# Kernel tuning notes

Hardware: AMD Instinct MI355X
Metric: run time of the kernel (lower is better)

Reference implementation:

```python
import jax, jax.numpy as jnp
import numpy as np

N_STREAMS = 4
DIM = 256
TMAX = 20
RMS_EPS = 1e-05
SK_EPS = 1e-08


def sinkhorn_knopp(logits):
    # logits: [B, T, n, n]; tmax fixed iterations of row/col normalization
    x = logits.astype(jnp.float32)
    x = x - jnp.max(x, axis=(-2, -1), keepdims=True)
    x = jnp.exp(x)
    for _ in range(TMAX):
        x = x / (jnp.sum(x, axis=-2, keepdims=True) + SK_EPS)
        x = x / (jnp.sum(x, axis=-1, keepdims=True) + SK_EPS)
    return x.astype(logits.dtype)


def setup_inputs() -> dict:
    key = jax.random.key(0)
    ks = jax.random.split(key, 5)
    B, T, n, C = 8, 4096, N_STREAMS, DIM
    nc = n * C
    x_streams = jax.random.normal(ks[0], (B, T, n, C), dtype=jnp.float32)
    scale = jnp.ones((nc,), dtype=jnp.float32)
    lim = 1.0 / np.sqrt(nc)
    w_pre = jax.random.uniform(ks[1], (n, nc), minval=-lim, maxval=lim, dtype=jnp.float32)
    w_post = jax.random.uniform(ks[2], (n, nc), minval=-lim, maxval=lim, dtype=jnp.float32)
    w_res = jax.random.uniform(ks[3], (n * n, nc), minval=-lim, maxval=lim, dtype=jnp.float32)
    return {
        "x_streams": x_streams,
        "scale": scale,
        "w_pre": w_pre,
        "w_post": w_post,
        "w_res": w_res,
        "alpha_pre": jnp.float32(0.01),
        "alpha_post": jnp.float32(0.01),
        "alpha_res": jnp.float32(0.01),
        "b_pre": jnp.zeros((n,), dtype=jnp.float32),
        "b_post": jnp.zeros((n,), dtype=jnp.float32),
        "b_res": jnp.zeros((n * n,), dtype=jnp.float32),
    }


def reference(x_streams, scale, w_pre, w_post, w_res,
              alpha_pre, alpha_post, alpha_res, b_pre, b_post, b_res):
    B, T, n, C = x_streams.shape
    x_flat = x_streams.reshape(B, T, n * C)
    # RMSNorm over flattened stream dim
    rms = jnp.mean(x_flat * x_flat, axis=-1, keepdims=True)
    x_norm = x_flat * jax.lax.rsqrt(rms + RMS_EPS) * scale
    # routing projections (Linear with no bias == x @ W.T)
    h_pre = jax.nn.sigmoid(alpha_pre * (x_norm @ w_pre.T) + b_pre)          # [B,T,n]
    h_post = 2.0 * jax.nn.sigmoid(alpha_post * (x_norm @ w_post.T) + b_post)  # [B,T,n]
    h_res = (alpha_res * (x_norm @ w_res.T) + b_res).reshape(B, T, n, n)
    h_res = sinkhorn_knopp(h_res)
    # mixing
    x_in = jnp.einsum('btn,btnc->btc', h_pre, x_streams)   # pre-mix (residual = Identity)
    y = x_in
    resmix = jnp.einsum('btij,btjc->btic', h_res, x_streams)
    addy = h_post[..., None] * y[..., None, :]
    return resmix + addy
```

## Files before the change

kernel.cpp:

```cpp
#include <hip/hip_runtime.h>
#include <math.h>

#define G 16

__device__ __forceinline__ float sigmoidf_(float s) {
    return 1.0f / (1.0f + __expf(-s));
}

__device__ __forceinline__ float fold_(float X, float Y, int m, int l) {
    const bool hi = (l & m) != 0;
    const float a = hi ? Y : X;
    const float b = hi ? X : Y;
    return a + __shfl_xor(b, m);
}

__global__ __launch_bounds__(256, 2)
void fused_route_mix(const float* __restrict__ x,
                     const float* __restrict__ scale,
                     const float* __restrict__ w_pre,
                     const float* __restrict__ w_post,
                     const float* __restrict__ w_res,
                     const float* __restrict__ ap_p,
                     const float* __restrict__ apo_p,
                     const float* __restrict__ ar_p,
                     const float* __restrict__ b_pre,
                     const float* __restrict__ b_post,
                     const float* __restrict__ b_res,
                     float* __restrict__ out,
                     int rounds)
{
    __shared__ __align__(16) float xs[G * 1024];
    __shared__ float hraw[G * 24];
    __shared__ float sslds[G];
    __shared__ __align__(16) float Mlds[G * 16];

    const int t = threadIdx.x;
    const int w = t >> 6;
    const int l = t & 63;

    float wreg[6][16];
    {
        float scl[16];
        #pragma unroll
        for (int mp = 0; mp < 4; ++mp) {
            #pragma unroll
            for (int j = 0; j < 4; ++j)
                scl[4 * mp + j] = scale[4 * l + 256 * mp + j];
        }
        #pragma unroll
        for (int rr = 0; rr < 6; ++rr) {
            const int k = 6 * w + rr;
            const float* wp = (k < 4) ? (w_pre + (size_t)k * 1024)
                            : (k < 8) ? (w_post + (size_t)(k - 4) * 1024)
                                      : (w_res + (size_t)(k - 8) * 1024);
            #pragma unroll
            for (int mp = 0; mp < 4; ++mp)
                #pragma unroll
                for (int j = 0; j < 4; ++j)
                    wreg[rr][4 * mp + j] = wp[4 * l + 256 * mp + j] * scl[4 * mp + j];
        }
    }

    const float a_pre = ap_p[0], a_post = apo_p[0], a_res = ar_p[0];

    const int rstep = gridDim.x;

    float4 pf[G];
    {
        const float4* __restrict__ xg =
            (const float4*)(x + (size_t)blockIdx.x * (G * 1024));
        #pragma unroll
        for (int i = 0; i < G; ++i) pf[i] = xg[i * 256 + t];
    }

    for (int r = blockIdx.x; r < rounds; r += rstep) {
        const size_t base = (size_t)r * (G * 1024);
        float4* xs4 = (float4*)xs;

        #pragma unroll
        for (int i = 0; i < G; ++i)
            xs4[i * 256 + t] = pf[i];
        __syncthreads();

        const int rn = r + rstep;
        if (rn < rounds) {
            const float4* __restrict__ xg =
                (const float4*)(x + (size_t)rn * (G * 1024));
            #pragma unroll
            for (int i = 0; i < G; ++i) pf[i] = xg[i * 256 + t];
        }

        for (int i = 0; i < G; ++i) {
            float p0 = 0.f, p1 = 0.f, p2 = 0.f, p3 = 0.f, p4 = 0.f, p5 = 0.f;
            float ss = 0.f;
            const float4* __restrict__ xi4 = (const float4*)(xs + i * 1024);
            #pragma unroll
            for (int mp = 0; mp < 4; ++mp) {
                const float4 xv = xi4[l + 64 * mp];
                const float xe[4] = {xv.x, xv.y, xv.z, xv.w};
                #pragma unroll
                for (int j = 0; j < 4; ++j) {
                    const float xj = xe[j];
                    p0 = fmaf(xj, wreg[0][4 * mp + j], p0);
                    p1 = fmaf(xj, wreg[1][4 * mp + j], p1);
                    p2 = fmaf(xj, wreg[2][4 * mp + j], p2);
                    p3 = fmaf(xj, wreg[3][4 * mp + j], p3);
                    p4 = fmaf(xj, wreg[4][4 * mp + j], p4);
                    p5 = fmaf(xj, wreg[5][4 * mp + j], p5);
                    ss = fmaf(xj, xj, ss);
                }
            }
            const float q0 = fold_(p0, p1, 32, l);
            const float q1 = fold_(p2, p3, 32, l);
            const float q2 = fold_(p4, p5, 32, l);
            const float q3 = ss + __shfl_xor(ss, 32);
            const float r0v = fold_(q0, q1, 16, l);
            const float r1v = fold_(q2, q3, 16, l);
            float s = fold_(r0v, r1v, 8, l);
            s += __shfl_xor(s, 4);
            s += __shfl_xor(s, 2);
            s += __shfl_xor(s, 1);
            if ((l & 7) == 0) {
                const int vid = ((l >> 3) & 1) * 4 + ((l >> 4) & 1) * 2 + ((l >> 5) & 1);
                if (vid < 6) hraw[i * 24 + 6 * w + vid] = s;
                else if (w == 0 && vid == 6) sslds[i] = s;
            }
        }
        __syncthreads();

        if (t < G) {
            const int tk = t;
            const float inv = rsqrtf(sslds[tk] * (1.0f / 1024.0f) + 1e-5f);
            float hr[24];
            #pragma unroll
            for (int k = 0; k < 24; ++k) hr[k] = hraw[tk * 24 + k];

            float hpre[4], hpost[4];
            #pragma unroll
            for (int j = 0; j < 4; ++j)
                hpre[j] = sigmoidf_(fmaf(a_pre * inv, hr[j], b_pre[j]));
            #pragma unroll
            for (int i = 0; i < 4; ++i)
                hpost[i] = 2.0f * sigmoidf_(fmaf(a_post * inv, hr[4 + i], b_post[i]));

            float K[4][4];
            float mx = -1e30f;
            #pragma unroll
            for (int i = 0; i < 4; ++i) {
                #pragma unroll
                for (int j = 0; j < 4; ++j) {
                    const float vv = fmaf(a_res * inv, hr[8 + 4 * i + j], b_res[4 * i + j]);
                    K[i][j] = vv;
                    mx = fmaxf(mx, vv);
                }
            }
            #pragma unroll
            for (int i = 0; i < 4; ++i)
                #pragma unroll
                for (int j = 0; j < 4; ++j)
                    K[i][j] = __expf(K[i][j] - mx);

            float u[4] = {1.f, 1.f, 1.f, 1.f};
            float v[4] = {1.f, 1.f, 1.f, 1.f};
            for (int it = 0; it < 20; ++it) {
                #pragma unroll
                for (int j = 0; j < 4; ++j) {
                    const float S = u[0] * K[0][j] + u[1] * K[1][j]
                                  + u[2] * K[2][j] + u[3] * K[3][j];
                    v[j] = v[j] * __builtin_amdgcn_rcpf(fmaf(v[j], S, 1e-8f));
                }
                #pragma unroll
                for (int i = 0; i < 4; ++i) {
                    const float T = K[i][0] * v[0] + K[i][1] * v[1]
                                  + K[i][2] * v[2] + K[i][3] * v[3];
                    u[i] = u[i] * __builtin_amdgcn_rcpf(fmaf(u[i], T, 1e-8f));
                }
            }
            #pragma unroll
            for (int i = 0; i < 4; ++i)
                #pragma unroll
                for (int j = 0; j < 4; ++j)
                    Mlds[tk * 16 + 4 * i + j] =
                        fmaf(u[i] * K[i][j], v[j], hpost[i] * hpre[j]);
        }
        __syncthreads();

        for (int i = 0; i < G; ++i) {
            const float4 m4 = ((const float4*)Mlds)[i * 4 + w];
            const float4* xt = xs4 + i * 256;
            const float4 a0 = xt[0 * 64 + l];
            const float4 a1 = xt[1 * 64 + l];
            const float4 a2 = xt[2 * 64 + l];
            const float4 a3 = xt[3 * 64 + l];
            float4 o;
            o.x = m4.x * a0.x + m4.y * a1.x + m4.z * a2.x + m4.w * a3.x;
            o.y = m4.x * a0.y + m4.y * a1.y + m4.z * a2.y + m4.w * a3.y;
            o.z = m4.x * a0.z + m4.y * a1.z + m4.z * a2.z + m4.w * a3.z;
            o.w = m4.x * a0.w + m4.y * a1.w + m4.z * a2.w + m4.w * a3.w;
            ((float4*)(out + base))[i * 256 + w * 64 + l] = o;
        }
        __syncthreads();
    }
}

extern "C" void kernel_launch(void* const* d_in, const int* in_sizes, int n_in,
                              void* d_out, int out_size, void* d_ws, size_t ws_size,
                              hipStream_t stream) {
    const float* x      = (const float*)d_in[0];
    const float* scale  = (const float*)d_in[1];
    const float* w_pre  = (const float*)d_in[2];
    const float* w_post = (const float*)d_in[3];
    const float* w_res  = (const float*)d_in[4];
    const float* a_pre  = (const float*)d_in[5];
    const float* a_post = (const float*)d_in[6];
    const float* a_res  = (const float*)d_in[7];
    const float* b_pre  = (const float*)d_in[8];
    const float* b_post = (const float*)d_in[9];
    const float* b_res  = (const float*)d_in[10];
    float* out = (float*)d_out;

    const int tokens = in_sizes[0] / 1024;
    const int rounds = tokens / G;
    const int grid = rounds < 512 ? rounds : 512;

    fused_route_mix<<<grid, 256, 0, stream>>>(
        x, scale, w_pre, w_post, w_res,
        a_pre, a_post, a_res, b_pre, b_post, b_res,
        out, rounds);
}
```

Baseline: 308.7 us.

## Double-buffer token tiles via direct global-to-LDS loads and drop mix barriers

```diff
diff --git a/kernel.cpp b/kernel.cpp
--- a/kernel.cpp
+++ b/kernel.cpp
@@ -1,7 +1,7 @@
 #include <hip/hip_runtime.h>
 #include <math.h>
 
-#define G 16
+#define G 8
 
 __device__ __forceinline__ float sigmoidf_(float s) {
     return 1.0f / (1.0f + __expf(-s));
@@ -14,7 +14,14 @@
     return a + __shfl_xor(b, m);
 }
 
-__global__ __launch_bounds__(256, 2)
+__device__ __forceinline__ void gll16(const float4* g, float* lds) {
+    __builtin_amdgcn_global_load_lds(
+        (const __attribute__((address_space(1))) void*)g,
+        (__attribute__((address_space(3))) void*)lds, 16, 0, 0);
+}
+
+__global__ __launch_bounds__(256)
+__attribute__((amdgpu_waves_per_eu(2, 2)))
 void fused_route_mix(const float* __restrict__ x,
                      const float* __restrict__ scale,
                      const float* __restrict__ w_pre,
@@ -29,10 +36,9 @@
                      float* __restrict__ out,
                      int rounds)
 {
-    __shared__ __align__(16) float xs[G * 1024];
-    __shared__ float hraw[G * 24];
+    __shared__ __align__(16) float xs[2][G * 1024];
+    __shared__ __align__(16) float hraw[G * 24];
     __shared__ float sslds[G];
-    __shared__ __align__(16) float Mlds[G * 16];
 
     const int t = threadIdx.x;
     const int w = t >> 6;
@@ -42,11 +48,10 @@
     {
         float scl[16];
         #pragma unroll
-        for (int mp = 0; mp < 4; ++mp) {
+        for (int mp = 0; mp < 4; ++mp)
             #pragma unroll
             for (int j = 0; j < 4; ++j)
                 scl[4 * mp + j] = scale[4 * l + 256 * mp + j];
-        }
         #pragma unroll
         for (int rr = 0; rr < 6; ++rr) {
             const int k = 6 * w + rr;
@@ -62,24 +67,26 @@
     }
 
     const float a_pre = ap_p[0], a_post = apo_p[0], a_res = ar_p[0];
+    float bp[4], bpo[4], br[16];
+    #pragma unroll
+    for (int k = 0; k < 4; ++k) { bp[k] = b_pre[k]; bpo[k] = b_post[k]; }
+    #pragma unroll
+    for (int k = 0; k < 16; ++k) br[k] = b_res[k];
 
     const int rstep = gridDim.x;
-
-    float4 pf[G];
+    int cur = 0;
+
     {
         const float4* __restrict__ xg =
             (const float4*)(x + (size_t)blockIdx.x * (G * 1024));
         #pragma unroll
-        for (int i = 0; i < G; ++i) pf[i] = xg[i * 256 + t];
+        for (int i = 0; i < G; ++i)
+            gll16(xg + i * 256 + (w << 6) + l, &xs[0][i * 1024 + (w << 8)]);
     }
 
     for (int r = blockIdx.x; r < rounds; r += rstep) {
         const size_t base = (size_t)r * (G * 1024);
-        float4* xs4 = (float4*)xs;
-
-        #pragma unroll
-        for (int i = 0; i < G; ++i)
-            xs4[i * 256 + t] = pf[i];
+
         __syncthreads();
 
         const int rn = r + rstep;
@@ -87,13 +94,16 @@
             const float4* __restrict__ xg =
                 (const float4*)(x + (size_t)rn * (G * 1024));
             #pragma unroll
-            for (int i = 0; i < G; ++i) pf[i] = xg[i * 256 + t];
-        }
+            for (int i = 0; i < G; ++i)
+                gll16(xg + i * 256 + (w << 6) + l, &xs[cur ^ 1][i * 1024 + (w << 8)]);
+        }
+
+        const float* __restrict__ xb = xs[cur];
 
         for (int i = 0; i < G; ++i) {
             float p0 = 0.f, p1 = 0.f, p2 = 0.f, p3 = 0.f, p4 = 0.f, p5 = 0.f;
             float ss = 0.f;
-            const float4* __restrict__ xi4 = (const float4*)(xs + i * 1024);
+            const float4* __restrict__ xi4 = (const float4*)(xb + i * 1024);
             #pragma unroll
             for (int mp = 0; mp < 4; ++mp) {
                 const float4 xv = xi4[l + 64 * mp];
@@ -126,34 +136,40 @@
                 else if (w == 0 && vid == 6) sslds[i] = s;
             }
         }
-        __syncthreads();
-
-        if (t < G) {
-            const int tk = t;
+
+        asm volatile("s_waitcnt lgkmcnt(0)\n\ts_barrier" ::: "memory");
+
+        float Mw0, Mw1, Mw2, Mw3;
+        {
+            const int tk = l & (G - 1);
             const float inv = rsqrtf(sslds[tk] * (1.0f / 1024.0f) + 1e-5f);
             float hr[24];
-            #pragma unroll
-            for (int k = 0; k < 24; ++k) hr[k] = hraw[tk * 24 + k];
+            const float4* __restrict__ hp = (const float4*)(hraw + tk * 24);
+            #pragma unroll
+            for (int q = 0; q < 6; ++q) {
+                const float4 hv = hp[q];
+                hr[4 * q + 0] = hv.x; hr[4 * q + 1] = hv.y;
+                hr[4 * q + 2] = hv.z; hr[4 * q + 3] = hv.w;
+            }
 
             float hpre[4], hpost[4];
             #pragma unroll
             for (int j = 0; j < 4; ++j)
-                hpre[j] = sigmoidf_(fmaf(a_pre * inv, hr[j], b_pre[j]));
+                hpre[j] = sigmoidf_(fmaf(a_pre * inv, hr[j], bp[j]));
             #pragma unroll
             for (int i = 0; i < 4; ++i)
-                hpost[i] = 2.0f * sigmoidf_(fmaf(a_post * inv, hr[4 + i], b_post[i]));
+                hpost[i] = 2.0f * sigmoidf_(fmaf(a_post * inv, hr[4 + i], bpo[i]));
 
             float K[4][4];
             float mx = -1e30f;
             #pragma unroll
-            for (int i = 0; i < 4; ++i) {
+            for (int i = 0; i < 4; ++i)
                 #pragma unroll
                 for (int j = 0; j < 4; ++j) {
-                    const float vv = fmaf(a_res * inv, hr[8 + 4 * i + j], b_res[4 * i + j]);
+                    const float vv = fmaf(a_res * inv, hr[8 + 4 * i + j], br[4 * i + j]);
                     K[i][j] = vv;
                     mx = fmaxf(mx, vv);
                 }
-            }
             #pragma unroll
             for (int i = 0; i < 4; ++i)
                 #pragma unroll
@@ -176,30 +192,37 @@
                     u[i] = u[i] * __builtin_amdgcn_rcpf(fmaf(u[i], T, 1e-8f));
                 }
             }
-            #pragma unroll
-            for (int i = 0; i < 4; ++i)
-                #pragma unroll
-                for (int j = 0; j < 4; ++j)
-                    Mlds[tk * 16 + 4 * i + j] =
-                        fmaf(u[i] * K[i][j], v[j], hpost[i] * hpre[j]);
-        }
-        __syncthreads();
+
+            const float uw  = (w == 0) ? u[0] : (w == 1) ? u[1] : (w == 2) ? u[2] : u[3];
+            const float hpw = (w == 0) ? hpost[0] : (w == 1) ? hpost[1]
+                            : (w == 2) ? hpost[2] : hpost[3];
+            #define KW(j) ((w == 0) ? K[0][j] : (w == 1) ? K[1][j] : (w == 2) ? K[2][j] : K[3][j])
+            Mw0 = fmaf(uw * KW(0), v[0], hpw * hpre[0]);
+            Mw1 = fmaf(uw * KW(1), v[1], hpw * hpre[1]);
+            Mw2 = fmaf(uw * KW(2), v[2], hpw * hpre[2]);
+            Mw3 = fmaf(uw * KW(3), v[3], hpw * hpre[3]);
+            #undef KW
+        }
 
         for (int i = 0; i < G; ++i) {
-            const float4 m4 = ((const float4*)Mlds)[i * 4 + w];
-            const float4* xt = xs4 + i * 256;
+            const float m0 = __shfl(Mw0, i);
+            const float m1 = __shfl(Mw1, i);
+            const float m2 = __shfl(Mw2, i);
+            const float m3 = __shfl(Mw3, i);
+            const float4* __restrict__ xt = (const float4*)(xb + i * 1024);
             const float4 a0 = xt[0 * 64 + l];
             const float4 a1 = xt[1 * 64 + l];
             const float4 a2 = xt[2 * 64 + l];
             const float4 a3 = xt[3 * 64 + l];
             float4 o;
-            o.x = m4.x * a0.x + m4.y * a1.x + m4.z * a2.x + m4.w * a3.x;
-            o.y = m4.x * a0.y + m4.y * a1.y + m4.z * a2.y + m4.w * a3.y;
-            o.z = m4.x * a0.z + m4.y * a1.z + m4.z * a2.z + m4.w * a3.z;
-            o.w = m4.x * a0.w + m4.y * a1.w + m4.z * a2.w + m4.w * a3.w;
-            ((float4*)(out + base))[i * 256 + w * 64 + l] = o;
-        }
-        __syncthreads();
+            o.x = m0 * a0.x + m1 * a1.x + m2 * a2.x + m3 * a3.x;
+            o.y = m0 * a0.y + m1 * a1.y + m2 * a2.y + m3 * a3.y;
+            o.z = m0 * a0.z + m1 * a1.z + m2 * a2.z + m3 * a3.z;
+            o.w = m0 * a0.w + m1 * a1.w + m2 * a2.w + m3 * a3.w;
+            ((float4*)(out + base))[i * 256 + (w << 6) + l] = o;
+        }
+
+        cur ^= 1;
     }
 }
 
```

Measured after the change: 293.0 us. 5.1% less time.
